# Optimization experiments

Measured on AMD Instinct MI355X. Metric: run time of the kernel, lower is better.

Reference implementation:

```python
import jax, jax.numpy as jnp
import numpy as np

C = 512
HEADS = 4
GROUPS = 32
EPS = 1e-6


def setup_inputs() -> dict:
    key = jax.random.key(0)
    ks = jax.random.split(key, 6)
    s = 1.0 / np.sqrt(C)
    return {
        "x": jax.random.normal(ks[0], (2, C, 64, 64), dtype=jnp.float32),
        "gn_scale": jnp.ones((C,), jnp.float32),
        "gn_bias": jnp.zeros((C,), jnp.float32),
        "wq": jax.random.normal(ks[1], (C, C), jnp.float32) * s,
        "bq": jnp.zeros((C,), jnp.float32),
        "wk": jax.random.normal(ks[2], (C, C), jnp.float32) * s,
        "bk": jnp.zeros((C,), jnp.float32),
        "wv": jax.random.normal(ks[3], (C, C), jnp.float32) * s,
        "bv": jnp.zeros((C,), jnp.float32),
        "wo": jax.random.normal(ks[4], (C, C), jnp.float32) * s,
        "bo": jnp.zeros((C,), jnp.float32),
    }


def group_norm(x, scale, bias):
    # x: [b, c, h, w]; GroupNorm with 32 groups, eps 1e-6, affine
    b, c, h, w = x.shape
    xg = x.reshape(b, GROUPS, c // GROUPS, h, w)
    mean = jnp.mean(xg, axis=(2, 3, 4), keepdims=True)
    var = jnp.var(xg, axis=(2, 3, 4), keepdims=True)
    xg = (xg - mean) * jax.lax.rsqrt(var + EPS)
    x = xg.reshape(b, c, h, w)
    return x * scale[None, :, None, None] + bias[None, :, None, None]


def conv1x1(x, w, b):
    # 1x1 conv == per-pixel linear: [b,c,h,w] x [o,c] -> [b,o,h,w]
    return jnp.einsum('bchw,oc->bohw', x, w) + b[None, :, None, None]


def reference(x, gn_scale, gn_bias, wq, bq, wk, bk, wv, bv, wo, bo):
    b, c, h, w = x.shape
    hc = c // HEADS
    n = h * w

    h_ = group_norm(x, gn_scale, gn_bias)
    q = conv1x1(h_, wq, bq).reshape(b, HEADS, hc, n)
    k = conv1x1(h_, wk, bk).reshape(b, HEADS, hc, n)
    v = conv1x1(h_, wv, bv).reshape(b, HEADS, hc, n)

    # NOTE: scale uses full channel count c (repo quirk), not head_channel
    scale = jnp.asarray(c, x.dtype) ** -0.5
    scores = jnp.einsum('bhcn,bhcm->bhnm', q, k) * scale  # [b,H,N,N]
    attn = jax.nn.softmax(scores, axis=-1)
    out = jnp.einsum('bhnm,bhcm->bhcn', attn, v)  # [b,H,hc,N]

    out = out.reshape(b, c, h, w)
    return x + conv1x1(out, wo, bo)
```

## Files before the change

kernel.cpp:

```cpp
#include <hip/hip_runtime.h>

typedef float    f32x4 __attribute__((ext_vector_type(4)));
typedef short    bf16x8 __attribute__((ext_vector_type(8)));
typedef unsigned short u16;
typedef u16      u16x4 __attribute__((ext_vector_type(4)));
typedef unsigned u32;
typedef u32      u32x4 __attribute__((ext_vector_type(4)));

#define MFMA16(a, b, c) __builtin_amdgcn_mfma_f32_16x16x32_bf16((a), (b), (c), 0, 0, 0)

#define CCH 512
#define NPIX 4096
#define NHEAD 4
#define HC 128
#define NSPLIT 2
#define KVCHUNK (NPIX / NSPLIT)
#define QK_SCALE 0.04419417382415922f
#define LOG2E 1.4426950408889634f

__device__ __forceinline__ u16 f2b(float f) {
  unsigned u = __builtin_bit_cast(unsigned, f);
  u += 0x7FFFu + ((u >> 16) & 1u);
  return (u16)(u >> 16);
}
__device__ __forceinline__ float b2f(u16 b) {
  return __builtin_bit_cast(float, ((unsigned)b) << 16);
}

__device__ __forceinline__ void gl_lds16(const u16* g, u16* l) {
  __builtin_amdgcn_global_load_lds((const __attribute__((address_space(1))) void*)g,
                                   (__attribute__((address_space(3))) void*)l, 16, 0, 0);
}

__global__ void wconv_k(const float* __restrict__ w0, const float* __restrict__ w1,
                        const float* __restrict__ w2, const float* __restrict__ w3,
                        u16* __restrict__ dst) {
  int m = blockIdx.y;
  const float* src = (m == 0) ? w0 : (m == 1) ? w1 : (m == 2) ? w2 : w3;
  int i = (blockIdx.x * 256 + threadIdx.x) * 4;
  f32x4 v = *(const f32x4*)(src + i);
  u16x4 o = { f2b(v[0]), f2b(v[1]), f2b(v[2]), f2b(v[3]) };
  *(u16x4*)(dst + (size_t)m * (CCH * CCH) + i) = o;
}

__global__ void gn_stats_k(const float* __restrict__ x, float* __restrict__ pstats) {
  int blk = blockIdx.x;
  const f32x4* p = (const f32x4*)(x + (size_t)blk * 16384);
  int t = threadIdx.x, wv = t >> 6, l = t & 63;
  float s = 0.f, ss = 0.f;
  for (int i = t; i < 4096; i += 256) {
    f32x4 v = p[i];
    s  += v[0] + v[1] + v[2] + v[3];
    ss += v[0]*v[0] + v[1]*v[1] + v[2]*v[2] + v[3]*v[3];
  }
  #pragma unroll
  for (int d = 32; d; d >>= 1) { s += __shfl_down(s, d, 64); ss += __shfl_down(ss, d, 64); }
  __shared__ float red[8];
  if (l == 0) { red[wv*2] = s; red[wv*2+1] = ss; }
  __syncthreads();
  if (t == 0) {
    pstats[blk*2]   = red[0] + red[2] + red[4] + red[6];
    pstats[blk*2+1] = red[1] + red[3] + red[5] + red[7];
  }
}

__global__ void gn_norm_k(const float* __restrict__ x, const float* __restrict__ gns,
                          const float* __restrict__ gnb, const float* __restrict__ pstats,
                          u16* __restrict__ Ht) {
  int t = threadIdx.x;
  int ct = blockIdx.x * 64, nt = blockIdx.y * 64, b = blockIdx.z;
  int c0 = ct + (t & 15) * 4;
  int n0 = nt + (t >> 4) * 4;
  const float* xb = x + ((size_t)b * CCH + c0) * NPIX + n0;
  int g = b * 32 + (c0 >> 4);
  const f32x4* ps = (const f32x4*)(pstats + g * 8);
  f32x4 p0 = ps[0], p1 = ps[1];
  float s  = p0[0] + p0[2] + p1[0] + p1[2];
  float ss = p0[1] + p0[3] + p1[1] + p1[3];
  float mean = s * (1.f/65536.f);
  float var  = ss * (1.f/65536.f) - mean*mean;
  float rstd = rsqrtf(var + 1e-6f);
  f32x4 rows[4];
  #pragma unroll
  for (int j = 0; j < 4; ++j) {
    f32x4 v = *(const f32x4*)(xb + (size_t)j * NPIX);
    float a  = rstd * gns[c0 + j];
    float bb = gnb[c0 + j] - mean * a;
    rows[j] = v * a + bb;
  }
  #pragma unroll
  for (int i = 0; i < 4; ++i) {
    u16x4 o = { f2b(rows[0][i]), f2b(rows[1][i]), f2b(rows[2][i]), f2b(rows[3][i]) };
    *(u16x4*)(Ht + ((size_t)b * NPIX + n0 + i) * CCH + c0) = o;
  }
}

template<int MODE>
__global__ __launch_bounds__(256) void gemm_nt(const u16* __restrict__ A,
                                               const u16* __restrict__ B,
                                               const float* __restrict__ bias,
                                               const float* __restrict__ bias2,
                                               u16* __restrict__ outb,
                                               u16* __restrict__ outb2,
                                               float* __restrict__ outf,
                                               const float* __restrict__ resid,
                                               float alpha) {
  __shared__ __align__(16) u16 As[128 * 32];
  __shared__ __align__(16) u16 Bs[128 * 32];
  const int t = threadIdx.x, l = t & 63, wv = t >> 6;
  const int l16 = l & 15, lq = l >> 4;
  const int mt = blockIdx.x * 128, nt = blockIdx.y * 128, z = blockIdx.z;
  const u16* Ap = A + (size_t)mt * CCH;
  const u16* Bp = (MODE == 3) ? (B + (size_t)nt * CCH)
                              : (B + ((size_t)z * NPIX + nt) * CCH);
  const int wm = (wv >> 1) * 64, wn = (wv & 1) * 64;
  f32x4 acc[4][4] = {};
  for (int k0 = 0; k0 < CCH; k0 += 32) {
    __syncthreads();
    #pragma unroll
    for (int j = 0; j < 2; ++j) {
      int idx = t + j * 256;
      int row = idx >> 2, kc = (idx & 3) * 8;
      gl_lds16(Ap + (size_t)row * CCH + k0 + kc, As + idx * 8);
      gl_lds16(Bp + (size_t)row * CCH + k0 + kc, Bs + idx * 8);
    }
    __syncthreads();
    bf16x8 af[4], bfr[4];
    #pragma unroll
    for (int i = 0; i < 4; ++i) {
      af[i]  = *(const bf16x8*)(As + (wm + i * 16 + l16) * 32 + lq * 8);
      bfr[i] = *(const bf16x8*)(Bs + (wn + i * 16 + l16) * 32 + lq * 8);
    }
    #pragma unroll
    for (int mi = 0; mi < 4; ++mi)
      #pragma unroll
      for (int ni = 0; ni < 4; ++ni)
        acc[mi][ni] = MFMA16(af[mi], bfr[ni], acc[mi][ni]);
  }
  #pragma unroll
  for (int mi = 0; mi < 4; ++mi)
    #pragma unroll
    for (int ni = 0; ni < 4; ++ni)
      #pragma unroll
      for (int r = 0; r < 4; ++r) {
        int grow = mt + wm + mi * 16 + lq * 4 + r;
        int gcol = nt + wn + ni * 16 + l16;
        float v = acc[mi][ni][r];
        if (MODE == 1) {
          outb[((size_t)z * CCH + grow) * NPIX + gcol] = f2b(v + bias[grow]);
        } else if (MODE == 2) {
          size_t off = ((size_t)z * CCH + grow) * NPIX + gcol;
          outf[off] = v + bias[grow] + resid[off];
        } else {
          if (gcol < 512)
            outb[(size_t)grow * CCH + gcol] = f2b((v + bias[gcol]) * alpha);
          else
            outb2[(size_t)grow * CCH + (gcol - 512)] = f2b(v + bias2[gcol - 512]);
        }
      }
}

__global__ __launch_bounds__(256, 2) void flash_k(const u16* __restrict__ Qt,
                                                  const u16* __restrict__ Kt,
                                                  const u16* __restrict__ Vc,
                                                  u16* __restrict__ sl0, u16* __restrict__ sl1,
                                                  float* __restrict__ mlp) {
  __shared__ __align__(16) char lds[65536];
  const int t = threadIdx.x, wv = t >> 6, l = t & 63;
  const int l16 = l & 15, lq = l >> 4;
  const int orig = blockIdx.x;
  const int gid = (orig & 7) * 64 + (orig >> 3);
  const int qx = gid & 31, grp = gid >> 5;
  const int hd = grp & 3, b = (grp >> 2) & 1, s = grp >> 3;
  const int qt0 = qx * 128 + wv * 32;

  const u16* Q = Qt + ((size_t)b * NPIX + qt0) * CCH + hd * HC;
  const u16* Kbase = Kt + (size_t)b * NPIX * CCH + hd * HC;
  const u16* Vbase = Vc + (size_t)b * CCH * NPIX + (size_t)hd * HC * NPIX;
  u16* slab = (s == 0) ? sl0 : sl1;
  u16* Ob = slab + ((size_t)(b * NHEAD + hd) * NPIX + qt0) * HC;
  size_t mlR0 = (size_t)s * 32768 + (size_t)(b * NHEAD + hd) * NPIX + qt0;

  bf16x8 qf[2][4];
  #pragma unroll
  for (int mi = 0; mi < 2; ++mi)
    #pragma unroll
    for (int kk = 0; kk < 4; ++kk)
      qf[mi][kk] = *(const bf16x8*)(Q + (size_t)(mi * 16 + l16) * CCH + kk * 32 + lq * 8);

  const int m_beg = s * KVCHUNK;
  const int sw = (l16 & 7) << 4;
  const int vb2 = (lq & 1) * 32 + (lq >> 1) * 16;

  int kbase[4], vbase[2];
  #pragma unroll
  for (int kk = 0; kk < 4; ++kk) kbase[kk] = l16 * 256 + ((kk * 64 + lq * 16) ^ sw);
  #pragma unroll
  for (int ks = 0; ks < 2; ++ks) vbase[ks] = 32768 + l16 * 128 + ((ks * 64 + vb2) ^ sw);

  u32 kgo[4], vgo[4];
  #pragma unroll
  for (int j = 0; j < 4; ++j) {
    int g = j * 256 + t;
    { int row = g >> 4, src = ((g & 15) << 4) ^ ((row & 7) << 4);
      kgo[j] = (u32)row * CCH + (src >> 1); }
    { int row = g >> 3, src = ((g & 7) << 4) ^ ((row & 7) << 4);
      vgo[j] = (u32)row * NPIX + (src >> 1); }
  }

  const short one_bf = (short)0x3F80;
  const bf16x8 vones = { one_bf, one_bf, one_bf, one_bf, one_bf, one_bf, one_bf, one_bf };

  f32x4 oacc[2][8] = {};
  f32x4 osum[2] = {};

  {
    const u16* kg = Kbase + (size_t)m_beg * CCH;
    const u16* vg = Vbase + m_beg;
    #pragma unroll
    for (int j = 0; j < 4; ++j) {
      gl_lds16(kg + kgo[j], (u16*)lds + (j * 256 + t) * 8);
      gl_lds16(vg + vgo[j], (u16*)(lds + 32768) + (j * 256 + t) * 8);
    }
  }
  asm volatile("s_waitcnt vmcnt(0)" ::: "memory");
  __syncthreads();

  const int NT = KVCHUNK / 64;

#define FLASH_BODY(CUR, M0, DOSTAGE)                                                   \
  {                                                                                    \
    if (DOSTAGE) {                                                                     \
      const u16* kg = Kbase + (size_t)((M0) + 64) * CCH;                               \
      const u16* vg = Vbase + ((M0) + 64);                                             \
      _Pragma("unroll")                                                                \
      for (int j = 0; j < 4; ++j) {                                                    \
        gl_lds16(kg + kgo[j], (u16*)(lds + ((CUR) ^ 1) * 16384) + (j * 256 + t) * 8);  \
        gl_lds16(vg + vgo[j], (u16*)(lds + 32768 + ((CUR) ^ 1) * 16384) + (j * 256 + t) * 8); \
      }                                                                                \
    }                                                                                  \
    f32x4 S[2][4] = {};                                                                \
    __builtin_amdgcn_s_setprio(1);                                                     \
    _Pragma("unroll")                                                                  \
    for (int kk = 0; kk < 4; ++kk)                                                     \
      _Pragma("unroll")                                                                \
      for (int mm = 0; mm < 4; ++mm) {                                                 \
        bf16x8 kf = *(const bf16x8*)(lds + kbase[kk] + mm * 4096 + (CUR) * 16384);     \
        S[0][mm] = MFMA16(kf, qf[0][kk], S[0][mm]);                                    \
        S[1][mm] = MFMA16(kf, qf[1][kk], S[1][mm]);                                    \
      }                                                                                \
    __builtin_amdgcn_s_setprio(0);                                                     \
    u32 pk[2][4][2];                                                                   \
    _Pragma("unroll")                                                                  \
    for (int mi = 0; mi < 2; ++mi) {                                                   \
      _Pragma("unroll")                                                                \
      for (int mm = 0; mm < 4; ++mm) {                                                 \
        f32x4 p;                                                                       \
        _Pragma("unroll")                                                              \
        for (int r = 0; r < 4; ++r) p[r] = exp2f(S[mi][mm][r]);                        \
        asm("v_cvt_pk_bf16_f32 %0, %1, %2" : "=v"(pk[mi][mm][0]) : "v"(p[0]), "v"(p[1])); \
        asm("v_cvt_pk_bf16_f32 %0, %1, %2" : "=v"(pk[mi][mm][1]) : "v"(p[2]), "v"(p[3])); \
      }                                                                                \
    }                                                                                  \
    bf16x8 pa[2][2];                                                                   \
    _Pragma("unroll")                                                                  \
    for (int mi = 0; mi < 2; ++mi)                                                     \
      _Pragma("unroll")                                                                \
      for (int ks = 0; ks < 2; ++ks) {                                                 \
        u32 a0 = pk[mi][2 * ks][0], a1 = pk[mi][2 * ks][1];                            \
        u32 b0 = pk[mi][2 * ks + 1][0], b1 = pk[mi][2 * ks + 1][1];                    \
        asm("v_permlane16_swap_b32 %0, %1" : "+v"(a0), "+v"(b0));                      \
        asm("v_permlane16_swap_b32 %0, %1" : "+v"(a1), "+v"(b1));                      \
        u32x4 w = { a0, a1, b0, b1 };                                                  \
        pa[mi][ks] = __builtin_bit_cast(bf16x8, w);                                    \
      }                                                                                \
    __builtin_amdgcn_s_setprio(1);                                                     \
    _Pragma("unroll")                                                                  \
    for (int ks = 0; ks < 2; ++ks) {                                                   \
      osum[0] = MFMA16(pa[0][ks], vones, osum[0]);                                     \
      osum[1] = MFMA16(pa[1][ks], vones, osum[1]);                                     \
      _Pragma("unroll")                                                                \
      for (int cc = 0; cc < 8; ++cc) {                                                 \
        bf16x8 vf = *(const bf16x8*)(lds + vbase[ks] + cc * 2048 + (CUR) * 16384);     \
        oacc[0][cc] = MFMA16(pa[0][ks], vf, oacc[0][cc]);                              \
        oacc[1][cc] = MFMA16(pa[1][ks], vf, oacc[1][cc]);                              \
      }                                                                                \
    }                                                                                  \
    __builtin_amdgcn_s_setprio(0);                                                     \
    asm volatile("s_waitcnt vmcnt(0)" ::: "memory");                                   \
    __syncthreads();                                                                   \
  }

  for (int it = 0; it < NT; it += 2) {
    FLASH_BODY(0, m_beg + it * 64, true)
    FLASH_BODY(1, m_beg + it * 64 + 64, (it + 2 < NT))
  }
#undef FLASH_BODY

  #pragma unroll
  for (int mi = 0; mi < 2; ++mi)
    #pragma unroll
    for (int cc = 0; cc < 8; ++cc)
      #pragma unroll
      for (int r = 0; r < 4; ++r)
        Ob[(size_t)(mi * 16 + lq * 4 + r) * HC + cc * 16 + l16] = f2b(oacc[mi][cc][r]);
  if (l16 == 0) {
    #pragma unroll
    for (int mi = 0; mi < 2; ++mi)
      #pragma unroll
      for (int r = 0; r < 4; ++r)
        mlp[mlR0 + mi * 16 + lq * 4 + r] = osum[mi][r];
  }
}

__global__ void merge_k(const u16* __restrict__ s0, const u16* __restrict__ s1,
                        const float* __restrict__ ml, u16* __restrict__ Ot) {
  int t = threadIdx.x;
  int R = blockIdx.x * 32 + (t >> 3);
  int ch = (t & 7) * 16;
  float L = ml[R] + ml[32768 + R];
  float inv = 1.f / L;
  float acc[16] = {};
  const u16* sp[2] = { s0, s1 };
  #pragma unroll
  for (int s = 0; s < 2; ++s) {
    const bf16x8* p = (const bf16x8*)(sp[s] + (size_t)R * HC + ch);
    #pragma unroll
    for (int j = 0; j < 2; ++j) {
      bf16x8 v = p[j];
      #pragma unroll
      for (int e = 0; e < 8; ++e) acc[j * 8 + e] += b2f((u16)v[e]);
    }
  }
  int b = R >> 14, h = (R >> 12) & 3, q = R & 4095;
  u16* o = Ot + ((size_t)((b << 12) + q) * CCH) + h * HC + ch;
  #pragma unroll
  for (int j = 0; j < 4; ++j) {
    u16x4 o4 = { f2b(acc[j*4] * inv), f2b(acc[j*4+1] * inv),
                 f2b(acc[j*4+2] * inv), f2b(acc[j*4+3] * inv) };
    *(u16x4*)(o + j * 4) = o4;
  }
}

extern "C" void kernel_launch(void* const* d_in, const int* in_sizes, int n_in,
                              void* d_out, int out_size, void* d_ws, size_t ws_size,
                              hipStream_t stream) {
  const float* x   = (const float*)d_in[0];
  const float* gns = (const float*)d_in[1];
  const float* gnb = (const float*)d_in[2];
  const float* wq  = (const float*)d_in[3];
  const float* bq  = (const float*)d_in[4];
  const float* wk  = (const float*)d_in[5];
  const float* bk  = (const float*)d_in[6];
  const float* wv  = (const float*)d_in[7];
  const float* bv  = (const float*)d_in[8];
  const float* wo  = (const float*)d_in[9];
  const float* bo  = (const float*)d_in[10];
  float* out = (float*)d_out;
  char* ws = (char*)d_ws;

  u16*   wb    = (u16*)ws;
  u16*   Ht    = (u16*)(ws + (size_t)( 2u << 20));
  u16*   Qt    = (u16*)(ws + (size_t)(10u << 20));
  u16*   Kt    = (u16*)(ws + (size_t)(18u << 20));
  u16*   Vc    = (u16*)(ws + (size_t)(26u << 20));
  u16*   Ot    = (u16*)(ws + (size_t)(34u << 20));
  float* mlb   = (float*)(ws + (size_t)(42u << 20));
  float* stats = (float*)(ws + (size_t)(43u << 20));
  u16*   sl0   = Ht;
  u16*   sl1   = (u16*)d_out;

  wconv_k   <<<dim3(256, 4, 1), 256, 0, stream>>>(wq, wk, wv, wo, wb);
  gn_stats_k<<<dim3(256, 1, 1), 256, 0, stream>>>(x, stats);
  gn_norm_k <<<dim3(8, 64, 2),  256, 0, stream>>>(x, gns, gnb, stats, Ht);
  gemm_nt<3><<<dim3(64, 8, 1),  256, 0, stream>>>(Ht, wb, bq, bk, Qt, Kt, nullptr, nullptr,
                                                  QK_SCALE * LOG2E);
  gemm_nt<1><<<dim3(4, 32, 2),  256, 0, stream>>>(wb + 2u * 262144u, Ht, bv, nullptr, Vc, nullptr,
                                                  nullptr, nullptr, 1.0f);
  flash_k   <<<dim3(512, 1, 1), 256, 0, stream>>>(Qt, Kt, Vc, sl0, sl1, mlb);
  merge_k   <<<dim3(1024, 1, 1),256, 0, stream>>>(sl0, sl1, mlb, Ot);
  gemm_nt<2><<<dim3(4, 32, 2),  256, 0, stream>>>(wb + 3u * 262144u, Ot, bo, nullptr, nullptr,
                                                  nullptr, out, x, 1.0f);
}
```

Baseline: 156.3 us.

## Double-buffer GEMM LDS tiles and merge weight-convert with GN stats kernel

The projection GEMM now uses two LDS buffers, issuing the global-to-LDS loads for the next K slice before running the MFMAs on the current one, with one barrier per step instead of two. This is meant to hide global load latency behind compute. Separately, the weight bf16 conversion and the group-norm statistics kernels are merged into one launch to save a kernel launch. Doubling LDS per block may lower occupancy.

Result: no change. 153.5 us (-1.7%).

```diff
diff --git a/kernel.cpp b/kernel.cpp
--- a/kernel.cpp
+++ b/kernel.cpp
@@ -32,21 +32,23 @@
                                    (__attribute__((address_space(3))) void*)l, 16, 0, 0);
 }
 
-__global__ void wconv_k(const float* __restrict__ w0, const float* __restrict__ w1,
-                        const float* __restrict__ w2, const float* __restrict__ w3,
-                        u16* __restrict__ dst) {
-  int m = blockIdx.y;
-  const float* src = (m == 0) ? w0 : (m == 1) ? w1 : (m == 2) ? w2 : w3;
-  int i = (blockIdx.x * 256 + threadIdx.x) * 4;
-  f32x4 v = *(const f32x4*)(src + i);
-  u16x4 o = { f2b(v[0]), f2b(v[1]), f2b(v[2]), f2b(v[3]) };
-  *(u16x4*)(dst + (size_t)m * (CCH * CCH) + i) = o;
-}
-
-__global__ void gn_stats_k(const float* __restrict__ x, float* __restrict__ pstats) {
-  int blk = blockIdx.x;
-  const f32x4* p = (const f32x4*)(x + (size_t)blk * 16384);
-  int t = threadIdx.x, wv = t >> 6, l = t & 63;
+__global__ void prep_k(const float* __restrict__ w0, const float* __restrict__ w1,
+                       const float* __restrict__ w2, const float* __restrict__ w3,
+                       u16* __restrict__ dst,
+                       const float* __restrict__ x, float* __restrict__ pstats) {
+  int blk = blockIdx.x, t = threadIdx.x;
+  if (blk < 1024) {
+    int m = blk >> 8;
+    const float* src = (m == 0) ? w0 : (m == 1) ? w1 : (m == 2) ? w2 : w3;
+    int i = ((blk & 255) * 256 + t) * 4;
+    f32x4 v = *(const f32x4*)(src + i);
+    u16x4 o = { f2b(v[0]), f2b(v[1]), f2b(v[2]), f2b(v[3]) };
+    *(u16x4*)(dst + (size_t)m * (CCH * CCH) + i) = o;
+    return;
+  }
+  int sblk = blk - 1024;
+  const f32x4* p = (const f32x4*)(x + (size_t)sblk * 16384);
+  int wv = t >> 6, l = t & 63;
   float s = 0.f, ss = 0.f;
   for (int i = t; i < 4096; i += 256) {
     f32x4 v = p[i];
@@ -59,8 +61,8 @@
   if (l == 0) { red[wv*2] = s; red[wv*2+1] = ss; }
   __syncthreads();
   if (t == 0) {
-    pstats[blk*2]   = red[0] + red[2] + red[4] + red[6];
-    pstats[blk*2+1] = red[1] + red[3] + red[5] + red[7];
+    pstats[sblk*2]   = red[0] + red[2] + red[4] + red[6];
+    pstats[sblk*2+1] = red[1] + red[3] + red[5] + red[7];
   }
 }
 
@@ -105,8 +107,8 @@
                                                float* __restrict__ outf,
                                                const float* __restrict__ resid,
                                                float alpha) {
-  __shared__ __align__(16) u16 As[128 * 32];
-  __shared__ __align__(16) u16 Bs[128 * 32];
+  __shared__ __align__(16) u16 As[2][128 * 32];
+  __shared__ __align__(16) u16 Bs[2][128 * 32];
   const int t = threadIdx.x, l = t & 63, wv = t >> 6;
   const int l16 = l & 15, lq = l >> 4;
   const int mt = blockIdx.x * 128, nt = blockIdx.y * 128, z = blockIdx.z;
@@ -115,28 +117,49 @@
                               : (B + ((size_t)z * NPIX + nt) * CCH);
   const int wm = (wv >> 1) * 64, wn = (wv & 1) * 64;
   f32x4 acc[4][4] = {};
-  for (int k0 = 0; k0 < CCH; k0 += 32) {
-    __syncthreads();
-    #pragma unroll
-    for (int j = 0; j < 2; ++j) {
-      int idx = t + j * 256;
-      int row = idx >> 2, kc = (idx & 3) * 8;
-      gl_lds16(Ap + (size_t)row * CCH + k0 + kc, As + idx * 8);
-      gl_lds16(Bp + (size_t)row * CCH + k0 + kc, Bs + idx * 8);
-    }
-    __syncthreads();
-    bf16x8 af[4], bfr[4];
-    #pragma unroll
-    for (int i = 0; i < 4; ++i) {
-      af[i]  = *(const bf16x8*)(As + (wm + i * 16 + l16) * 32 + lq * 8);
-      bfr[i] = *(const bf16x8*)(Bs + (wn + i * 16 + l16) * 32 + lq * 8);
-    }
-    #pragma unroll
-    for (int mi = 0; mi < 4; ++mi)
-      #pragma unroll
-      for (int ni = 0; ni < 4; ++ni)
-        acc[mi][ni] = MFMA16(af[mi], bfr[ni], acc[mi][ni]);
-  }
+
+  #pragma unroll
+  for (int j = 0; j < 2; ++j) {
+    int idx = t + j * 256;
+    int row = idx >> 2, kc = (idx & 3) * 8;
+    gl_lds16(Ap + (size_t)row * CCH + kc, &As[0][0] + idx * 8);
+    gl_lds16(Bp + (size_t)row * CCH + kc, &Bs[0][0] + idx * 8);
+  }
+  asm volatile("s_waitcnt vmcnt(0)" ::: "memory");
+  __syncthreads();
+
+#define GEMM_BODY(CUR, K0, DOSTAGE)                                                   \
+  {                                                                                   \
+    if (DOSTAGE) {                                                                    \
+      _Pragma("unroll")                                                               \
+      for (int j = 0; j < 2; ++j) {                                                   \
+        int idx = t + j * 256;                                                        \
+        int row = idx >> 2, kc = (idx & 3) * 8;                                       \
+        gl_lds16(Ap + (size_t)row * CCH + (K0) + 32 + kc, &As[(CUR) ^ 1][0] + idx * 8); \
+        gl_lds16(Bp + (size_t)row * CCH + (K0) + 32 + kc, &Bs[(CUR) ^ 1][0] + idx * 8); \
+      }                                                                               \
+    }                                                                                 \
+    bf16x8 af[4], bfr[4];                                                             \
+    _Pragma("unroll")                                                                 \
+    for (int i = 0; i < 4; ++i) {                                                     \
+      af[i]  = *(const bf16x8*)(&As[CUR][0] + (wm + i * 16 + l16) * 32 + lq * 8);     \
+      bfr[i] = *(const bf16x8*)(&Bs[CUR][0] + (wn + i * 16 + l16) * 32 + lq * 8);     \
+    }                                                                                 \
+    _Pragma("unroll")                                                                 \
+    for (int mi = 0; mi < 4; ++mi)                                                    \
+      _Pragma("unroll")                                                               \
+      for (int ni = 0; ni < 4; ++ni)                                                  \
+        acc[mi][ni] = MFMA16(af[mi], bfr[ni], acc[mi][ni]);                           \
+    asm volatile("s_waitcnt vmcnt(0)" ::: "memory");                                  \
+    __syncthreads();                                                                  \
+  }
+
+  for (int k0 = 0; k0 < CCH; k0 += 64) {
+    GEMM_BODY(0, k0, true)
+    GEMM_BODY(1, k0 + 32, (k0 + 64 < CCH))
+  }
+#undef GEMM_BODY
+
   #pragma unroll
   for (int mi = 0; mi < 4; ++mi)
     #pragma unroll
@@ -370,8 +393,7 @@
   u16*   sl0   = Ht;
   u16*   sl1   = (u16*)d_out;
 
-  wconv_k   <<<dim3(256, 4, 1), 256, 0, stream>>>(wq, wk, wv, wo, wb);
-  gn_stats_k<<<dim3(256, 1, 1), 256, 0, stream>>>(x, stats);
+  prep_k    <<<dim3(1280, 1, 1), 256, 0, stream>>>(wq, wk, wv, wo, wb, x, stats);
   gn_norm_k <<<dim3(8, 64, 2),  256, 0, stream>>>(x, gns, gnb, stats, Ht);
   gemm_nt<3><<<dim3(64, 8, 1),  256, 0, stream>>>(Ht, wb, bq, bk, Qt, Kt, nullptr, nullptr,
                                                   QK_SCALE * LOG2E);
```
